# Kernel optimization log

Hardware: AMD Instinct MI355X
Metric: run time of the kernel (lower is better)

## Reference

```python
import jax, jax.numpy as jnp
import numpy as np

H = 2048      # hidden_size
I = 8192      # intermediate_size
NH = 16       # num_heads
HD = H // NH  # head_dim
EPS = 1e-6


def setup_inputs() -> dict:
    key = jax.random.key(0)
    ks = jax.random.split(key, 10)
    s = 0.02
    return {
        "hidden_states": jax.random.normal(ks[0], (2, 2048, H), dtype=jnp.float32),
        "wq": jax.random.normal(ks[1], (H, H), dtype=jnp.float32) * s,
        "wk": jax.random.normal(ks[2], (H, H), dtype=jnp.float32) * s,
        "wv": jax.random.normal(ks[3], (H, H), dtype=jnp.float32) * s,
        "wo": jax.random.normal(ks[4], (H, H), dtype=jnp.float32) * s,
        "w_gate": jax.random.normal(ks[5], (H, I), dtype=jnp.float32) * s,
        "w_up": jax.random.normal(ks[6], (H, I), dtype=jnp.float32) * s,
        "w_down": jax.random.normal(ks[7], (I, H), dtype=jnp.float32) * s,
        "ln1_w": jnp.ones((H,), dtype=jnp.float32),
        "ln2_w": jnp.ones((H,), dtype=jnp.float32),
    }


def rmsnorm(x, w):
    xf = x.astype(jnp.float32)
    var = jnp.mean(xf * xf, axis=-1, keepdims=True)
    return w * (xf * jax.lax.rsqrt(var + EPS)).astype(x.dtype)


def reference(hidden_states, wq, wk, wv, wo, w_gate, w_up, w_down, ln1_w, ln2_w):
    b, s, _ = hidden_states.shape
    residual = hidden_states
    x = rmsnorm(hidden_states, ln1_w)

    # attention (no RoPE, no causal mask, per source)
    q = (x @ wq).reshape(b, s, NH, HD)
    k = (x @ wk).reshape(b, s, NH, HD)
    v = (x @ wv).reshape(b, s, NH, HD)
    scores = jnp.einsum('bqhd,bkhd->bhqk', q, k) / jnp.sqrt(jnp.float32(HD))
    attn = jax.nn.softmax(scores, axis=-1)
    out = jnp.einsum('bhqk,bkhd->bqhd', attn, v).reshape(b, s, H)
    hidden = residual + out @ wo

    residual = hidden
    y = rmsnorm(hidden, ln2_w)
    gate = jax.nn.silu(y @ w_gate)
    up = y @ w_up
    return residual + (gate * up) @ w_down
```

## Files before the change

### kernel.cpp

```cpp
#include <hip/hip_runtime.h>
#include <hip/hip_bf16.h>

#define HDIM 2048
#define IDIM 8192
#define NHEADS 16
#define HEADD 128
#define BATCH 2
#define SEQ 2048
#define MTOK 4096

typedef unsigned short u16;
typedef __bf16 bf16x8 __attribute__((ext_vector_type(8)));
typedef float f32x4 __attribute__((ext_vector_type(4)));
typedef float f32x16 __attribute__((ext_vector_type(16)));
typedef unsigned short u16x8 __attribute__((ext_vector_type(8)));
typedef unsigned int u32x2 __attribute__((ext_vector_type(2)));
typedef unsigned int u32x4 __attribute__((ext_vector_type(4)));
typedef unsigned int uv2 __attribute__((ext_vector_type(2)));

__device__ __forceinline__ u16 f2b(float f) {
  unsigned u = __builtin_bit_cast(unsigned, f);
  u += 0x7FFFu + ((u >> 16) & 1u);
  return (u16)(u >> 16);
}
__device__ __forceinline__ float b2f(u16 b) {
  unsigned u = ((unsigned)b) << 16;
  return __builtin_bit_cast(float, u);
}
__device__ __forceinline__ void gl_lds16(const void* g, void* l) {
  auto gp = (const __attribute__((address_space(1))) unsigned int*)((unsigned long long)g);
  auto lp = (__attribute__((address_space(3))) unsigned int*)((unsigned)(unsigned long long)l);
  __builtin_amdgcn_global_load_lds(gp, lp, 16, 0, 0);
}
__device__ __forceinline__ unsigned cvtpk(float lo, float hi) {
  unsigned r;
  asm("v_cvt_pk_bf16_f32 %0, %1, %2" : "=v"(r) : "v"(lo), "v"(hi));
  return r;
}
__device__ __forceinline__ void rect_swz(int gx, int gy, int& bx, int& by) {
  const int bid = blockIdx.y * gx + blockIdx.x;
  const int xcd = bid & 7, ii = bid >> 3;
  const int j = ii & 31, rin = ii >> 5;
  const int rectIdx = rin * 8 + xcd;
  const int nry = gy >> 2;
  const int ry = rectIdx % nry, rx = rectIdx / nry;
  by = ry * 4 + (j >> 3);
  bx = rx * 8 + (j & 7);
}

__global__ __launch_bounds__(256) void wtrans_all(const float* __restrict__ wq, const float* __restrict__ wk,
                                                  const float* __restrict__ wv, const float* __restrict__ wo,
                                                  const float* __restrict__ wg, const float* __restrict__ wu,
                                                  const float* __restrict__ wd,
                                                  u16* __restrict__ wqkvT, u16* __restrict__ woT,
                                                  u16* __restrict__ wgT, u16* __restrict__ wuT,
                                                  u16* __restrict__ wdT) {
  int bidf = blockIdx.x;
  const float* W;
  u16* Wt;
  int K, N, rowoff, bx, by;
  if (bidf < 3072) {
    int s = bidf >> 10, r = bidf & 1023;
    W = s == 0 ? wq : (s == 1 ? wk : wv);
    Wt = wqkvT; K = 2048; N = 2048; rowoff = s * 2048;
    bx = r & 31; by = r >> 5;
  } else if (bidf < 4096) {
    int r = bidf - 3072;
    W = wo; Wt = woT; K = 2048; N = 2048; rowoff = 0;
    bx = r & 31; by = r >> 5;
  } else if (bidf < 8192) {
    int r = bidf - 4096;
    W = wg; Wt = wgT; K = 2048; N = 8192; rowoff = 0;
    bx = r & 127; by = r >> 7;
  } else if (bidf < 12288) {
    int r = bidf - 8192;
    W = wu; Wt = wuT; K = 2048; N = 8192; rowoff = 0;
    bx = r & 127; by = r >> 7;
  } else {
    int r = bidf - 12288;
    W = wd; Wt = wdT; K = 8192; N = 2048; rowoff = 0;
    bx = r & 31; by = r >> 5;
  }
  __shared__ float t[64][65];
  int n0 = bx * 64, k0 = by * 64;
  int tid = threadIdx.x;
  int kr = tid >> 4, nc = (tid & 15) * 4;
#pragma unroll
  for (int p = 0; p < 4; p++) {
    float4 v = *(const float4*)&W[(size_t)(k0 + p * 16 + kr) * N + n0 + nc];
    t[nc + 0][p * 16 + kr] = v.x;
    t[nc + 1][p * 16 + kr] = v.y;
    t[nc + 2][p * 16 + kr] = v.z;
    t[nc + 3][p * 16 + kr] = v.w;
  }
  __syncthreads();
  int n = tid >> 2, kq = (tid & 3) * 16;
  u16 tmp[16];
#pragma unroll
  for (int i = 0; i < 16; i++) tmp[i] = f2b(t[n][kq + i]);
  *(u16x8*)&Wt[(size_t)(rowoff + n0 + n) * K + k0 + kq] = *(u16x8*)&tmp[0];
  *(u16x8*)&Wt[(size_t)(rowoff + n0 + n) * K + k0 + kq + 8] = *(u16x8*)&tmp[8];
}

__global__ __launch_bounds__(256) void vtrans_k(const u16* __restrict__ qkv, u16* __restrict__ vt) {
  __shared__ u16 t[32][33];
  int s0 = blockIdx.x * 32, d0 = blockIdx.y * 32, bh = blockIdx.z;
  int b = bh >> 4, h = bh & 15;
  int tx = threadIdx.x, ty = threadIdx.y;
#pragma unroll
  for (int i = 0; i < 4; i++)
    t[ty + i * 8][tx] = qkv[(size_t)(b * SEQ + s0 + ty + i * 8) * 6144 + 4096 + h * HEADD + d0 + tx];
  __syncthreads();
#pragma unroll
  for (int i = 0; i < 4; i++)
    vt[(size_t)(bh * HEADD + d0 + ty + i * 8) * SEQ + s0 + tx] = t[tx][ty + i * 8];
}

__global__ __launch_bounds__(256) void rmsnorm_k(const float* __restrict__ X, const float* __restrict__ W,
                                                 u16* __restrict__ O) {
  int row = blockIdx.x;
  int tid = threadIdx.x;
  const float* x = X + (size_t)row * HDIM;
  float4 v0 = ((const float4*)x)[tid * 2];
  float4 v1 = ((const float4*)x)[tid * 2 + 1];
  float ss = v0.x * v0.x + v0.y * v0.y + v0.z * v0.z + v0.w * v0.w
           + v1.x * v1.x + v1.y * v1.y + v1.z * v1.z + v1.w * v1.w;
#pragma unroll
  for (int off = 32; off > 0; off >>= 1) ss += __shfl_down(ss, off);
  __shared__ float red[4];
  if ((tid & 63) == 0) red[tid >> 6] = ss;
  __syncthreads();
  float rs = rsqrtf((red[0] + red[1] + red[2] + red[3]) * (1.0f / HDIM) + 1e-6f);
  const float* w = W + tid * 8;
  u16* o = O + (size_t)row * HDIM + tid * 8;
  float vals[8] = {v0.x, v0.y, v0.z, v0.w, v1.x, v1.y, v1.z, v1.w};
#pragma unroll
  for (int j = 0; j < 8; j++) o[j] = f2b(w[j] * vals[j] * rs);
}

template <int EPI>
__global__ __launch_bounds__(512, 2) void gemm_lean(const u16* __restrict__ A, const u16* __restrict__ Bt,
                                                    int M, int N, int K,
                                                    u16* __restrict__ Cb, float* __restrict__ Cf,
                                                    const float* __restrict__ Res) {
  __shared__ char lds[98304];
  const int tid = threadIdx.x, lane = tid & 63, w = tid >> 6;
  const int wm = w >> 1, wn = w & 1;
  int bx, by;
  rect_swz(gridDim.x, gridDim.y, bx, by);
  const int m0 = by * 256, n0 = bx * 128;
  const int NT = K >> 6;

  const int srow = w * 8 + (lane >> 3);
  const int kko = ((lane & 7) ^ (lane >> 3)) * 8;
  const u16* Asrc = A + (size_t)(m0 + srow) * K + kko;
  const u16* Bsrc = Bt + (size_t)(n0 + srow) * K + kko;
  const int wofs = w * 1024;

#define SSA(buf, kt)                                                                          \
  {                                                                                           \
    gl_lds16(Asrc + (size_t)(kt) * 64, lds + (buf) * 49152 + wofs);                           \
    gl_lds16(Asrc + 64 * (size_t)K + (size_t)(kt) * 64, lds + (buf) * 49152 + 8192 + wofs);   \
    gl_lds16(Asrc + 128 * (size_t)K + (size_t)(kt) * 64, lds + (buf) * 49152 + 16384 + wofs); \
    gl_lds16(Asrc + 192 * (size_t)K + (size_t)(kt) * 64, lds + (buf) * 49152 + 24576 + wofs); \
  }
#define SSB(buf, kt)                                                                         \
  {                                                                                          \
    gl_lds16(Bsrc + (size_t)(kt) * 64, lds + (buf) * 49152 + 32768 + wofs);                  \
    gl_lds16(Bsrc + 64 * (size_t)K + (size_t)(kt) * 64, lds + (buf) * 49152 + 40960 + wofs); \
  }
#define LG0 { asm volatile("s_waitcnt lgkmcnt(0)" ::: "memory"); __builtin_amdgcn_sched_barrier(0); }

  const int l15 = lane & 15, l4 = lane >> 4;
  const int kq0 = ((l4) ^ (l15 & 7)) << 4;
  const int kq1 = ((4 + l4) ^ (l15 & 7)) << 4;
  const int abase = (wm * 64 + l15) * 128;
  const int bbase = 32768 + (wn * 64 + l15) * 128;

  const f32x4 fz = {0.f, 0.f, 0.f, 0.f};
  f32x4 acc[4][4];
#pragma unroll
  for (int i = 0; i < 4; i++)
#pragma unroll
    for (int jj = 0; jj < 4; jj++) acc[i][jj] = fz;
  bf16x8 af0[4], af1[4], b0[4], b1[4];

  SSA(0, 0);
  SSB(0, 0);
  asm volatile("s_waitcnt vmcnt(2)" ::: "memory");
  __builtin_amdgcn_s_barrier();

  for (int t = 0; t < NT; ++t) {
    const int buf = t & 1, nb = buf ^ 1;
    const char* Lb = lds + buf * 49152;
    const int t1 = (t + 1 < NT) ? t + 1 : NT - 1;
#pragma unroll
    for (int mf = 0; mf < 4; mf++) af0[mf] = *(const bf16x8*)(Lb + abase + mf * 2048 + kq0);
    SSA(nb, t1);
    asm volatile("s_waitcnt vmcnt(4)" ::: "memory");
    __builtin_amdgcn_s_barrier();
#pragma unroll
    for (int nf = 0; nf < 4; nf++) b0[nf] = *(const bf16x8*)(Lb + bbase + nf * 2048 + kq0);
    LG0;
    __builtin_amdgcn_s_setprio(1);
#pragma unroll
    for (int mf = 0; mf < 4; mf++)
#pragma unroll
      for (int nf = 0; nf < 4; nf++)
        acc[mf][nf] = __builtin_amdgcn_mfma_f32_16x16x32_bf16(af0[mf], b0[nf], acc[mf][nf], 0, 0, 0);
    __builtin_amdgcn_s_setprio(0);
#pragma unroll
    for (int mf = 0; mf < 4; mf++) af1[mf] = *(const bf16x8*)(Lb + abase + mf * 2048 + kq1);
#pragma unroll
    for (int nf = 0; nf < 4; nf++) b1[nf] = *(const bf16x8*)(Lb + bbase + nf * 2048 + kq1);
    SSB(nb, t1);
    asm volatile("s_waitcnt vmcnt(2)" ::: "memory");
    LG0;
    __builtin_amdgcn_s_barrier();
    __builtin_amdgcn_s_setprio(1);
#pragma unroll
    for (int mf = 0; mf < 4; mf++)
#pragma unroll
      for (int nf = 0; nf < 4; nf++)
        acc[mf][nf] = __builtin_amdgcn_mfma_f32_16x16x32_bf16(af1[mf], b1[nf], acc[mf][nf], 0, 0, 0);
    __builtin_amdgcn_s_setprio(0);
  }
  asm volatile("s_waitcnt vmcnt(0)" ::: "memory");

#pragma unroll
  for (int mf = 0; mf < 4; mf++) {
#pragma unroll
    for (int jr = 0; jr < 4; jr++) {
      const int m = m0 + wm * 64 + mf * 16 + l4 * 4 + jr;
#pragma unroll
      for (int nf = 0; nf < 4; nf++) {
        const int n = n0 + wn * 64 + nf * 16 + l15;
        float v = acc[mf][nf][jr];
        size_t idx = (size_t)m * N + n;
        if (EPI == 0) {
          Cb[idx] = f2b(v);
        } else {
          Cf[idx] = Res[idx] + v;
        }
      }
    }
  }
#undef SSA
#undef SSB
#undef LG0
}

__global__ __launch_bounds__(512, 2) void gemm_fgu2(const u16* __restrict__ A, const u16* __restrict__ Bg,
                                                    const u16* __restrict__ Bu, u16* __restrict__ G) {
  __shared__ char lds[131072];
  const int tid = threadIdx.x, lane = tid & 63, w = tid >> 6;
  const int wm = w >> 2, wn = w & 3;
  int bx, by;
  rect_swz(64, 16, bx, by);
  const int m0 = by * 256, n0 = bx * 128;
  const int NT = 32;

  const int srow = w * 8 + (lane >> 3);
  const int kko = ((lane & 7) ^ (lane >> 3)) * 8;
  const u16* Asrc = A + (size_t)(m0 + srow) * 2048 + kko;
  const u16* Bgsrc = Bg + (size_t)(n0 + srow) * 2048 + kko;
  const u16* Busrc = Bu + (size_t)(n0 + srow) * 2048 + kko;
  const int wofs = w * 1024;

#define SSA(buf, kt)                                                              \
  {                                                                               \
    gl_lds16(Asrc + (kt) * 64, lds + (buf) * 65536 + wofs);                       \
    gl_lds16(Asrc + 64 * 2048 + (kt) * 64, lds + (buf) * 65536 + 8192 + wofs);    \
    gl_lds16(Asrc + 128 * 2048 + (kt) * 64, lds + (buf) * 65536 + 16384 + wofs);  \
    gl_lds16(Asrc + 192 * 2048 + (kt) * 64, lds + (buf) * 65536 + 24576 + wofs);  \
  }
#define SBGU(buf, kt)                                                             \
  {                                                                               \
    gl_lds16(Bgsrc + (kt) * 64, lds + (buf) * 65536 + 32768 + wofs);              \
    gl_lds16(Bgsrc + 64 * 2048 + (kt) * 64, lds + (buf) * 65536 + 40960 + wofs);  \
    gl_lds16(Busrc + (kt) * 64, lds + (buf) * 65536 + 49152 + wofs);              \
    gl_lds16(Busrc + 64 * 2048 + (kt) * 64, lds + (buf) * 65536 + 57344 + wofs);  \
  }
#define LG0 { asm volatile("s_waitcnt lgkmcnt(0)" ::: "memory"); __builtin_amdgcn_sched_barrier(0); }

  const int l15 = lane & 15, l4 = lane >> 4;
  const int kq0 = ((l4) ^ (l15 & 7)) << 4;
  const int kq1 = ((4 + l4) ^ (l15 & 7)) << 4;
  const int abase = (wm * 128 + l15) * 128;
  const int gbase = 32768 + (wn * 32 + l15) * 128;
  const int ubase = 49152 + (wn * 32 + l15) * 128;

  const f32x4 fz = {0.f, 0.f, 0.f, 0.f};
  f32x4 ag[8][2], au[8][2];
#pragma unroll
  for (int i = 0; i < 8; i++)
#pragma unroll
    for (int jj = 0; jj < 2; jj++) { ag[i][jj] = fz; au[i][jj] = fz; }
  bf16x8 af0[8], af1[8], bg0[2], bg1[2], bu0[2], bu1[2];

  SSA(0, 0);
  SBGU(0, 0);
  asm volatile("s_waitcnt vmcnt(4)" ::: "memory");
  __builtin_amdgcn_s_barrier();

  for (int t = 0; t < NT; ++t) {
    const int buf = t & 1, nb = buf ^ 1;
    const char* Lb = lds + buf * 65536;
    const int t1 = (t + 1 < NT) ? t + 1 : NT - 1;
#pragma unroll
    for (int mf = 0; mf < 8; mf++) af0[mf] = *(const bf16x8*)(Lb + abase + mf * 2048 + kq0);
    SSA(nb, t1);
    asm volatile("s_waitcnt vmcnt(4)" ::: "memory");
    __builtin_amdgcn_s_barrier();
    bg0[0] = *(const bf16x8*)(Lb + gbase + kq0);
    bg0[1] = *(const bf16x8*)(Lb + gbase + 2048 + kq0);
    bu0[0] = *(const bf16x8*)(Lb + ubase + kq0);
    bu0[1] = *(const bf16x8*)(Lb + ubase + 2048 + kq0);
    bg1[0] = *(const bf16x8*)(Lb + gbase + kq1);
    bg1[1] = *(const bf16x8*)(Lb + gbase + 2048 + kq1);
    bu1[0] = *(const bf16x8*)(Lb + ubase + kq1);
    bu1[1] = *(const bf16x8*)(Lb + ubase + 2048 + kq1);
    LG0;
    __builtin_amdgcn_s_setprio(1);
#pragma unroll
    for (int mf = 0; mf < 8; mf++) {
      ag[mf][0] = __builtin_amdgcn_mfma_f32_16x16x32_bf16(af0[mf], bg0[0], ag[mf][0], 0, 0, 0);
      ag[mf][1] = __builtin_amdgcn_mfma_f32_16x16x32_bf16(af0[mf], bg0[1], ag[mf][1], 0, 0, 0);
      au[mf][0] = __builtin_amdgcn_mfma_f32_16x16x32_bf16(af0[mf], bu0[0], au[mf][0], 0, 0, 0);
      au[mf][1] = __builtin_amdgcn_mfma_f32_16x16x32_bf16(af0[mf], bu0[1], au[mf][1], 0, 0, 0);
    }
    __builtin_amdgcn_s_setprio(0);
#pragma unroll
    for (int mf = 0; mf < 8; mf++) af1[mf] = *(const bf16x8*)(Lb + abase + mf * 2048 + kq1);
    SBGU(nb, t1);
    asm volatile("s_waitcnt vmcnt(4)" ::: "memory");
    LG0;
    __builtin_amdgcn_s_barrier();
    __builtin_amdgcn_s_setprio(1);
#pragma unroll
    for (int mf = 0; mf < 8; mf++) {
      ag[mf][0] = __builtin_amdgcn_mfma_f32_16x16x32_bf16(af1[mf], bg1[0], ag[mf][0], 0, 0, 0);
      ag[mf][1] = __builtin_amdgcn_mfma_f32_16x16x32_bf16(af1[mf], bg1[1], ag[mf][1], 0, 0, 0);
      au[mf][0] = __builtin_amdgcn_mfma_f32_16x16x32_bf16(af1[mf], bu1[0], au[mf][0], 0, 0, 0);
      au[mf][1] = __builtin_amdgcn_mfma_f32_16x16x32_bf16(af1[mf], bu1[1], au[mf][1], 0, 0, 0);
    }
    __builtin_amdgcn_s_setprio(0);
  }
  asm volatile("s_waitcnt vmcnt(0)" ::: "memory");

#pragma unroll
  for (int mf = 0; mf < 8; mf++) {
#pragma unroll
    for (int jr = 0; jr < 4; jr++) {
      const int m = m0 + wm * 128 + mf * 16 + l4 * 4 + jr;
#pragma unroll
      for (int nf = 0; nf < 2; nf++) {
        const int n = n0 + wn * 32 + nf * 16 + l15;
        float g = ag[mf][nf][jr];
        float u = au[mf][nf][jr];
        float sg = g / (1.f + __expf(-g));
        G[(size_t)m * IDIM + n] = f2b(sg * u);
      }
    }
  }
#undef SSA
#undef SBGU
#undef LG0
}

__global__ __launch_bounds__(512, 2) void attn_k(const u16* __restrict__ qkv, const u16* __restrict__ vt,
                                                 u16* __restrict__ out) {
  __shared__ char Kl[2][16384];
  __shared__ char Vl[2][16384];
  int tid = threadIdx.x, lane = tid & 63, w = tid >> 6;
  int bid = blockIdx.y * 8 + blockIdx.x;
  int swz = (bid & 7) * 32 + (bid >> 3);
  int qb = swz & 7, bh = swz >> 3;
  int b = bh >> 4, h = bh & 15;
  int l31 = lane & 31, hi = lane >> 5;
  const float c = 0.088388347648318447f * 1.4426950408889634f;
  const float RT = 90.51f;

  const int qrow = qb * 256 + w * 32 + l31;
  bf16x8 q[8];
  {
    const u16* qp = qkv + (size_t)(b * SEQ + qrow) * 6144 + h * HEADD + hi * 8;
#pragma unroll
    for (int dt = 0; dt < 8; dt++) q[dt] = *(const bf16x8*)(qp + dt * 16);
  }
  f32x16 o[4];
#pragma unroll
  for (int i = 0; i < 4; i++)
#pragma unroll
    for (int j = 0; j < 16; j++) o[i][j] = 0.f;
  float mrow = -1e30f, lrow = 0.f;

#define ASTAGE(buf, t)                                                                     \
  {                                                                                        \
    int kv0_ = (t) * 64;                                                                   \
    _Pragma("unroll") for (int i = 0; i < 2; i++) {                                        \
      int r = w * 8 + i * 4 + (lane >> 4);                                                 \
      int col = ((lane & 15) ^ (r & 15)) * 8;                                              \
      const u16* src = qkv + (size_t)(b * SEQ + kv0_ + r) * 6144 + HDIM + h * HEADD + col; \
      gl_lds16(src, &Kl[buf][(w * 8 + i * 4) * 256]);                                      \
    }                                                                                      \
    _Pragma("unroll") for (int i = 0; i < 2; i++) {                                        \
      int d = w * 16 + i * 8 + (lane >> 3);                                                \
      int col = ((lane & 7) ^ (d & 7)) * 8;                                                \
      const u16* src = vt + (size_t)(bh * HEADD + d) * SEQ + kv0_ + col;                   \
      gl_lds16(src, &Vl[buf][(w * 16 + i * 8) * 128]);                                     \
    }                                                                                      \
  }

  ASTAGE(0, 0);
  __syncthreads();

  for (int t = 0; t < SEQ / 64; t++) {
    const int buf = t & 1;
    if (t + 1 < SEQ / 64) ASTAGE(buf ^ 1, t + 1);
    const char* Kb = &Kl[buf][0];
    const char* Vb = &Vl[buf][0];
    f32x16 s0, s1;
#pragma unroll
    for (int j = 0; j < 16; j++) { s0[j] = 0.f; s1[j] = 0.f; }
    const int ksl = l31 & 15;
    __builtin_amdgcn_s_setprio(1);
#pragma unroll
    for (int dt = 0; dt < 8; dt++) {
      bf16x8 k0 = *(const bf16x8*)(Kb + (l31)*256 + (((dt * 2 + hi) ^ ksl) << 4));
      bf16x8 k1 = *(const bf16x8*)(Kb + (32 + l31) * 256 + (((dt * 2 + hi) ^ ksl) << 4));
      s0 = __builtin_amdgcn_mfma_f32_32x32x16_bf16(k0, q[dt], s0, 0, 0, 0);
      s1 = __builtin_amdgcn_mfma_f32_32x32x16_bf16(k1, q[dt], s1, 0, 0, 0);
    }
    __builtin_amdgcn_s_setprio(0);
    float m8[8];
#pragma unroll
    for (int g = 0; g < 4; g++) {
      m8[g] = fmaxf(fmaxf(s0[4 * g], s0[4 * g + 1]), fmaxf(s0[4 * g + 2], s0[4 * g + 3]));
      m8[4 + g] = fmaxf(fmaxf(s1[4 * g], s1[4 * g + 1]), fmaxf(s1[4 * g + 2], s1[4 * g + 3]));
    }
    float vmax = fmaxf(fmaxf(fmaxf(m8[0], m8[1]), fmaxf(m8[2], m8[3])),
                       fmaxf(fmaxf(m8[4], m8[5]), fmaxf(m8[6], m8[7])));
    {
      uv2 pr = __builtin_amdgcn_permlane32_swap(__builtin_bit_cast(unsigned, vmax),
                                                __builtin_bit_cast(unsigned, vmax), false, false);
      vmax = fmaxf(__builtin_bit_cast(float, pr[0]), __builtin_bit_cast(float, pr[1]));
    }
    if (__any(vmax > mrow + RT)) {
      float mnew = fmaxf(mrow, vmax);
      float alpha = exp2f((mrow - mnew) * c);
      mrow = mnew;
      lrow *= alpha;
#pragma unroll
      for (int i = 0; i < 4; i++)
#pragma unroll
        for (int j = 0; j < 16; j++) o[i][j] *= alpha;
    }
    const float mc = mrow * c;
    float r4[4] = {0.f, 0.f, 0.f, 0.f};
#pragma unroll
    for (int j = 0; j < 16; j++) {
      s0[j] = exp2f(s0[j] * c - mc);
      r4[j & 3] += s0[j];
    }
#pragma unroll
    for (int j = 0; j < 16; j++) {
      s1[j] = exp2f(s1[j] * c - mc);
      r4[j & 3] += s1[j];
    }
    float rsum = (r4[0] + r4[1]) + (r4[2] + r4[3]);
    {
      uv2 pr = __builtin_amdgcn_permlane32_swap(__builtin_bit_cast(unsigned, rsum),
                                                __builtin_bit_cast(unsigned, rsum), false, false);
      rsum = __builtin_bit_cast(float, pr[0]) + __builtin_bit_cast(float, pr[1]);
    }
    lrow += rsum;
    bf16x8 pa[4];
#pragma unroll
    for (int half = 0; half < 2; half++) {
      const f32x16& sv = half ? s1 : s0;
#pragma unroll
      for (int blk = 0; blk < 2; blk++) {
        int base = blk * 8;
        unsigned A = cvtpk(sv[base + 0], sv[base + 1]);
        unsigned B = cvtpk(sv[base + 2], sv[base + 3]);
        unsigned C = cvtpk(sv[base + 4], sv[base + 5]);
        unsigned D = cvtpk(sv[base + 6], sv[base + 7]);
        uv2 ac = __builtin_amdgcn_permlane32_swap(A, C, false, false);
        uv2 bd = __builtin_amdgcn_permlane32_swap(B, D, false, false);
        u32x4 w4;
        w4[0] = ac[0]; w4[1] = bd[0]; w4[2] = ac[1]; w4[3] = bd[1];
        pa[half * 2 + blk] = __builtin_bit_cast(bf16x8, w4);
      }
    }
    __builtin_amdgcn_s_setprio(1);
#pragma unroll
    for (int dt4 = 0; dt4 < 4; dt4++) {
      const char* vbase = Vb + (dt4 * 32 + l31) * 128;
      const int vsl = l31 & 7;
#pragma unroll
      for (int ks = 0; ks < 4; ks++) {
        bf16x8 vb = *(const bf16x8*)(vbase + (((ks * 2 + hi) ^ vsl) << 4));
        o[dt4] = __builtin_amdgcn_mfma_f32_32x32x16_bf16(vb, pa[ks], o[dt4], 0, 0, 0);
      }
    }
    __builtin_amdgcn_s_setprio(0);
    __syncthreads();
  }
#undef ASTAGE

  const float linv = 1.0f / lrow;
  u16* orow = out + (size_t)(b * SEQ + qrow) * HDIM + h * HEADD;
#pragma unroll
  for (int dt4 = 0; dt4 < 4; dt4++) {
#pragma unroll
    for (int g = 0; g < 4; g++) {
      u32x2 st;
      st[0] = cvtpk(o[dt4][4 * g + 0] * linv, o[dt4][4 * g + 1] * linv);
      st[1] = cvtpk(o[dt4][4 * g + 2] * linv, o[dt4][4 * g + 3] * linv);
      *(u32x2*)(orow + dt4 * 32 + 8 * g + 4 * hi) = st;
    }
  }
}

extern "C" void kernel_launch(void* const* d_in, const int* in_sizes, int n_in,
                              void* d_out, int out_size, void* d_ws, size_t ws_size,
                              hipStream_t stream) {
  const float* hs  = (const float*)d_in[0];
  const float* wq  = (const float*)d_in[1];
  const float* wk  = (const float*)d_in[2];
  const float* wv  = (const float*)d_in[3];
  const float* wo  = (const float*)d_in[4];
  const float* wg  = (const float*)d_in[5];
  const float* wu  = (const float*)d_in[6];
  const float* wd  = (const float*)d_in[7];
  const float* ln1 = (const float*)d_in[8];
  const float* ln2 = (const float*)d_in[9];
  char* ws = (char*)d_ws;
  u16*   wqkvT = (u16*)(ws);
  u16*   woT   = (u16*)(ws + 25165824ull);
  u16*   wgT   = (u16*)(ws + 33554432ull);
  u16*   wuT   = (u16*)(ws + 67108864ull);
  u16*   wdT   = (u16*)(ws + 100663296ull);
  u16*   xb    = (u16*)(ws + 134217728ull);
  float* hid   = (float*)(ws + 150994944ull);
  u16*   qkv   = (u16*)(ws + 184549376ull);
  u16*   vtb   = (u16*)(ws + 234881024ull);
  u16*   attn  = (u16*)(ws + 251658368ull);
  u16*   g     = qkv;

  wtrans_all<<<16384, 256, 0, stream>>>(wq, wk, wv, wo, wg, wu, wd, wqkvT, woT, wgT, wuT, wdT);

  rmsnorm_k<<<MTOK, 256, 0, stream>>>(hs, ln1, xb);
  gemm_lean<0><<<dim3(48, 16), 512, 0, stream>>>(xb, wqkvT, MTOK, 6144, HDIM, qkv, nullptr, nullptr);
  vtrans_k<<<dim3(64, 4, 32), dim3(32, 8), 0, stream>>>(qkv, vtb);
  attn_k<<<dim3(8, 32), 512, 0, stream>>>(qkv, vtb, attn);
  gemm_lean<3><<<dim3(16, 16), 512, 0, stream>>>(attn, woT, MTOK, HDIM, HDIM, nullptr, hid, hs);
  rmsnorm_k<<<MTOK, 256, 0, stream>>>(hid, ln2, xb);
  gemm_fgu2<<<dim3(64, 16), 512, 0, stream>>>(xb, wgT, wuT, g);
  gemm_lean<3><<<dim3(16, 16), 512, 0, stream>>>(g, wdT, MTOK, HDIM, IDIM, nullptr, (float*)d_out, hid);
}
```

Before: 716.3 us.

## Split fused gate/up GEMM main loop into four interleaved load/compute phases

```diff
diff --git a/kernel.cpp b/kernel.cpp
--- a/kernel.cpp
+++ b/kernel.cpp
@@ -250,7 +250,7 @@
 #undef LG0
 }
 
-__global__ __launch_bounds__(512, 2) void gemm_fgu2(const u16* __restrict__ A, const u16* __restrict__ Bg,
+__global__ __launch_bounds__(512, 2) void gemm_fgu3(const u16* __restrict__ A, const u16* __restrict__ Bg,
                                                     const u16* __restrict__ Bu, u16* __restrict__ G) {
   __shared__ char lds[131072];
   const int tid = threadIdx.x, lane = tid & 63, w = tid >> 6;
@@ -267,17 +267,23 @@
   const u16* Busrc = Bu + (size_t)(n0 + srow) * 2048 + kko;
   const int wofs = w * 1024;
 
-#define SSA(buf, kt)                                                              \
+#define SA0H(buf, kt)                                                             \
   {                                                                               \
     gl_lds16(Asrc + (kt) * 64, lds + (buf) * 65536 + wofs);                       \
     gl_lds16(Asrc + 64 * 2048 + (kt) * 64, lds + (buf) * 65536 + 8192 + wofs);    \
+  }
+#define SA1H(buf, kt)                                                             \
+  {                                                                               \
     gl_lds16(Asrc + 128 * 2048 + (kt) * 64, lds + (buf) * 65536 + 16384 + wofs);  \
     gl_lds16(Asrc + 192 * 2048 + (kt) * 64, lds + (buf) * 65536 + 24576 + wofs);  \
   }
-#define SBGU(buf, kt)                                                             \
+#define SBG(buf, kt)                                                              \
   {                                                                               \
     gl_lds16(Bgsrc + (kt) * 64, lds + (buf) * 65536 + 32768 + wofs);              \
     gl_lds16(Bgsrc + 64 * 2048 + (kt) * 64, lds + (buf) * 65536 + 40960 + wofs);  \
+  }
+#define SBU(buf, kt)                                                              \
+  {                                                                               \
     gl_lds16(Busrc + (kt) * 64, lds + (buf) * 65536 + 49152 + wofs);              \
     gl_lds16(Busrc + 64 * 2048 + (kt) * 64, lds + (buf) * 65536 + 57344 + wofs);  \
   }
@@ -296,11 +302,13 @@
   for (int i = 0; i < 8; i++)
 #pragma unroll
     for (int jj = 0; jj < 2; jj++) { ag[i][jj] = fz; au[i][jj] = fz; }
-  bf16x8 af0[8], af1[8], bg0[2], bg1[2], bu0[2], bu1[2];
-
-  SSA(0, 0);
-  SBGU(0, 0);
-  asm volatile("s_waitcnt vmcnt(4)" ::: "memory");
+  bf16x8 af[8], bgf[2], buf2[2];
+
+  SA0H(0, 0);
+  SA1H(0, 0);
+  SBG(0, 0);
+  SBU(0, 0);
+  asm volatile("s_waitcnt vmcnt(2)" ::: "memory");
   __builtin_amdgcn_s_barrier();
 
   for (int t = 0; t < NT; ++t) {
@@ -308,43 +316,63 @@
     const char* Lb = lds + buf * 65536;
     const int t1 = (t + 1 < NT) ? t + 1 : NT - 1;
 #pragma unroll
-    for (int mf = 0; mf < 8; mf++) af0[mf] = *(const bf16x8*)(Lb + abase + mf * 2048 + kq0);
-    SSA(nb, t1);
-    asm volatile("s_waitcnt vmcnt(4)" ::: "memory");
-    __builtin_amdgcn_s_barrier();
-    bg0[0] = *(const bf16x8*)(Lb + gbase + kq0);
-    bg0[1] = *(const bf16x8*)(Lb + gbase + 2048 + kq0);
-    bu0[0] = *(const bf16x8*)(Lb + ubase + kq0);
-    bu0[1] = *(const bf16x8*)(Lb + ubase + 2048 + kq0);
-    bg1[0] = *(const bf16x8*)(Lb + gbase + kq1);
-    bg1[1] = *(const bf16x8*)(Lb + gbase + 2048 + kq1);
-    bu1[0] = *(const bf16x8*)(Lb + ubase + kq1);
-    bu1[1] = *(const bf16x8*)(Lb + ubase + 2048 + kq1);
+    for (int mf = 0; mf < 8; mf++) af[mf] = *(const bf16x8*)(Lb + abase + mf * 2048 + kq0);
+    bgf[0] = *(const bf16x8*)(Lb + gbase + kq0);
+    bgf[1] = *(const bf16x8*)(Lb + gbase + 2048 + kq0);
+    SA0H(nb, t1);
+    __builtin_amdgcn_s_barrier();
     LG0;
     __builtin_amdgcn_s_setprio(1);
 #pragma unroll
     for (int mf = 0; mf < 8; mf++) {
-      ag[mf][0] = __builtin_amdgcn_mfma_f32_16x16x32_bf16(af0[mf], bg0[0], ag[mf][0], 0, 0, 0);
-      ag[mf][1] = __builtin_amdgcn_mfma_f32_16x16x32_bf16(af0[mf], bg0[1], ag[mf][1], 0, 0, 0);
-      au[mf][0] = __builtin_amdgcn_mfma_f32_16x16x32_bf16(af0[mf], bu0[0], au[mf][0], 0, 0, 0);
-      au[mf][1] = __builtin_amdgcn_mfma_f32_16x16x32_bf16(af0[mf], bu0[1], au[mf][1], 0, 0, 0);
-    }
-    __builtin_amdgcn_s_setprio(0);
-#pragma unroll
-    for (int mf = 0; mf < 8; mf++) af1[mf] = *(const bf16x8*)(Lb + abase + mf * 2048 + kq1);
-    SBGU(nb, t1);
-    asm volatile("s_waitcnt vmcnt(4)" ::: "memory");
+      ag[mf][0] = __builtin_amdgcn_mfma_f32_16x16x32_bf16(af[mf], bgf[0], ag[mf][0], 0, 0, 0);
+      ag[mf][1] = __builtin_amdgcn_mfma_f32_16x16x32_bf16(af[mf], bgf[1], ag[mf][1], 0, 0, 0);
+    }
+    __builtin_amdgcn_s_setprio(0);
+    asm volatile("s_waitcnt vmcnt(2)" ::: "memory");
+    __builtin_amdgcn_s_barrier();
+    buf2[0] = *(const bf16x8*)(Lb + ubase + kq0);
+    buf2[1] = *(const bf16x8*)(Lb + ubase + 2048 + kq0);
+    SA1H(nb, t1);
+    __builtin_amdgcn_s_barrier();
     LG0;
-    __builtin_amdgcn_s_barrier();
     __builtin_amdgcn_s_setprio(1);
 #pragma unroll
     for (int mf = 0; mf < 8; mf++) {
-      ag[mf][0] = __builtin_amdgcn_mfma_f32_16x16x32_bf16(af1[mf], bg1[0], ag[mf][0], 0, 0, 0);
-      ag[mf][1] = __builtin_amdgcn_mfma_f32_16x16x32_bf16(af1[mf], bg1[1], ag[mf][1], 0, 0, 0);
-      au[mf][0] = __builtin_amdgcn_mfma_f32_16x16x32_bf16(af1[mf], bu1[0], au[mf][0], 0, 0, 0);
-      au[mf][1] = __builtin_amdgcn_mfma_f32_16x16x32_bf16(af1[mf], bu1[1], au[mf][1], 0, 0, 0);
-    }
-    __builtin_amdgcn_s_setprio(0);
+      au[mf][0] = __builtin_amdgcn_mfma_f32_16x16x32_bf16(af[mf], buf2[0], au[mf][0], 0, 0, 0);
+      au[mf][1] = __builtin_amdgcn_mfma_f32_16x16x32_bf16(af[mf], buf2[1], au[mf][1], 0, 0, 0);
+    }
+    __builtin_amdgcn_s_setprio(0);
+    __builtin_amdgcn_s_barrier();
+#pragma unroll
+    for (int mf = 0; mf < 8; mf++) af[mf] = *(const bf16x8*)(Lb + abase + mf * 2048 + kq1);
+    bgf[0] = *(const bf16x8*)(Lb + gbase + kq1);
+    bgf[1] = *(const bf16x8*)(Lb + gbase + 2048 + kq1);
+    SBG(nb, t1);
+    __builtin_amdgcn_s_barrier();
+    LG0;
+    __builtin_amdgcn_s_setprio(1);
+#pragma unroll
+    for (int mf = 0; mf < 8; mf++) {
+      ag[mf][0] = __builtin_amdgcn_mfma_f32_16x16x32_bf16(af[mf], bgf[0], ag[mf][0], 0, 0, 0);
+      ag[mf][1] = __builtin_amdgcn_mfma_f32_16x16x32_bf16(af[mf], bgf[1], ag[mf][1], 0, 0, 0);
+    }
+    __builtin_amdgcn_s_setprio(0);
+    __builtin_amdgcn_s_barrier();
+    buf2[0] = *(const bf16x8*)(Lb + ubase + kq1);
+    buf2[1] = *(const bf16x8*)(Lb + ubase + 2048 + kq1);
+    SBU(nb, t1);
+    __builtin_amdgcn_s_barrier();
+    LG0;
+    __builtin_amdgcn_s_setprio(1);
+#pragma unroll
+    for (int mf = 0; mf < 8; mf++) {
+      au[mf][0] = __builtin_amdgcn_mfma_f32_16x16x32_bf16(af[mf], buf2[0], au[mf][0], 0, 0, 0);
+      au[mf][1] = __builtin_amdgcn_mfma_f32_16x16x32_bf16(af[mf], buf2[1], au[mf][1], 0, 0, 0);
+    }
+    __builtin_amdgcn_s_setprio(0);
+    asm volatile("s_waitcnt vmcnt(2)" ::: "memory");
+    __builtin_amdgcn_s_barrier();
   }
   asm volatile("s_waitcnt vmcnt(0)" ::: "memory");
 
@@ -363,8 +391,10 @@
       }
     }
   }
-#undef SSA
-#undef SBGU
+#undef SA0H
+#undef SA1H
+#undef SBG
+#undef SBU
 #undef LG0
 }
 
@@ -557,6 +587,6 @@
   attn_k<<<dim3(8, 32), 512, 0, stream>>>(qkv, vtb, attn);
   gemm_lean<3><<<dim3(16, 16), 512, 0, stream>>>(attn, woT, MTOK, HDIM, HDIM, nullptr, hid, hs);
   rmsnorm_k<<<MTOK, 256, 0, stream>>>(hid, ln2, xb);
-  gemm_fgu2<<<dim3(64, 16), 512, 0, stream>>>(xb, wgT, wuT, g);
+  gemm_fgu3<<<dim3(64, 16), 512, 0, stream>>>(xb, wgT, wuT, g);
   gemm_lean<3><<<dim3(16, 16), 512, 0, stream>>>(g, wdT, MTOK, HDIM, IDIM, nullptr, (float*)d_out, hid);
 }
```

New measurement: 725.7 us. Within noise of the previous version (+1.3%).
